# Kernel tuning notes

Measured on AMD Instinct MI355X. Metric: run time of the kernel, lower is better.

## Reference

```python
import jax, jax.numpy as jnp
import numpy as np

H = 16  # num_heads


def rope_cos_sin(S, d):
    # interleaved RoPE tables: cos = [cos0,cos0,cos1,cos1,...], sin likewise
    pos = jnp.arange(S, dtype=jnp.float32)[:, None]            # [S,1]
    ids = jnp.arange(d // 2, dtype=jnp.float32)
    theta = jnp.power(10000.0, -2.0 * ids / d)                  # [d/2]
    ang = pos * theta                                           # [S,d/2]
    cos = jnp.repeat(jnp.cos(ang), 2, axis=-1)                  # [S,d]
    sin = jnp.repeat(jnp.sin(ang), 2, axis=-1)                  # [S,d]
    return cos, sin


def apply_rope(x, cos, sin):
    # x: [B,H,S,d]; x2 = [-x1, x0, -x3, x2, ...]
    x2 = jnp.stack([-x[..., 1::2], x[..., ::2]], axis=-1).reshape(x.shape)
    return x * cos + x2 * sin


def setup_inputs() -> dict:
    key = jax.random.key(0)
    ks = jax.random.split(key, 9)
    B, S, D = 2, 2048, 1024
    sc = 1.0 / np.sqrt(D)
    return {
        "x": jax.random.normal(ks[0], (B, S, D), dtype=jnp.float32),
        "Wq": jax.random.normal(ks[1], (D, D), dtype=jnp.float32) * sc,
        "bq": jnp.zeros((D,), dtype=jnp.float32),
        "Wk": jax.random.normal(ks[2], (D, D), dtype=jnp.float32) * sc,
        "bk": jnp.zeros((D,), dtype=jnp.float32),
        "Wv": jax.random.normal(ks[3], (D, D), dtype=jnp.float32) * sc,
        "bv": jnp.zeros((D,), dtype=jnp.float32),
        "Wo": jax.random.normal(ks[4], (D, D), dtype=jnp.float32) * sc,
        "bo": jnp.zeros((D,), dtype=jnp.float32),
    }


def reference(x, Wq, bq, Wk, bk, Wv, bv, Wo, bo):
    B, S, D = x.shape
    dk = D // H
    scale = dk ** -0.5  # lsa=False -> fixed scale
    # QKV projections -> [B,H,S,dk]
    q = (x @ Wq + bq).reshape(B, S, H, dk).transpose(0, 2, 1, 3)
    k = (x @ Wk + bk).reshape(B, S, H, dk).transpose(0, 2, 1, 3)
    v = (x @ Wv + bv).reshape(B, S, H, dk).transpose(0, 2, 1, 3)
    cos, sin = rope_cos_sin(S, dk)
    q = apply_rope(q, cos, sin)
    k = apply_rope(k, cos, sin)
    attn_scores = jnp.einsum('bhqd,bhkd->bhqk', q, k) * scale
    attn_weights = jax.nn.softmax(attn_scores, axis=-1)  # dropout p=0
    out = jnp.einsum('bhqk,bhkd->bhqd', attn_weights, v)
    out = out.transpose(0, 2, 1, 3).reshape(B, S, D)
    out = out @ Wo + bo
    return out, attn_weights
```

## Files before the change

### kernel.cpp

```cpp
#include <hip/hip_runtime.h>

typedef __attribute__((ext_vector_type(4))) float f32x4;
typedef __attribute__((ext_vector_type(4))) int   i32x4;
typedef __attribute__((ext_vector_type(8))) short bf16x8;
typedef __attribute__((ext_vector_type(4))) short s16x4;

#define HD 16
#define SQ 2048
#define DM 1024
#define DK 64
#define QSCALE 0.18033688011112042f

__device__ __forceinline__ short f2bf(float f){
  union { float f; unsigned u; } c; c.f = f;
  unsigned r = (c.u + 0x7FFFu + ((c.u >> 16) & 1u)) >> 16;
  return (short)r;
}
__device__ __forceinline__ f32x4 mfma16(bf16x8 a, bf16x8 b, f32x4 c){
  return __builtin_amdgcn_mfma_f32_16x16x32_bf16(a, b, c, 0, 0, 0);
}
__device__ __forceinline__ void gload16(const void* g, void* l){
  __builtin_amdgcn_global_load_lds(
      (const __attribute__((address_space(1))) unsigned*)g,
      (__attribute__((address_space(3))) unsigned*)l, 16, 0, 0);
}


__global__ void k_rope_tab(float2* __restrict__ tab){
  int i = blockIdx.x * 256 + threadIdx.x;
  int s = i >> 5, d2 = i & 31;
  float theta = powf(10000.0f, -(float)d2 / 32.0f);
  float ang = (float)s * theta;
  tab[i] = make_float2(cosf(ang), sinf(ang));
}

__global__ void k_cast(const float* __restrict__ x, short* __restrict__ xb){
  int i = (blockIdx.x * 256 + threadIdx.x) * 4;
  f32x4 v = *(const f32x4*)(x + i);
  s16x4 o;
  o[0] = f2bf(v[0]); o[1] = f2bf(v[1]); o[2] = f2bf(v[2]); o[3] = f2bf(v[3]);
  *(s16x4*)(xb + i) = o;
}

__global__ void k_wt4(const float* __restrict__ W0, const float* __restrict__ W1,
                      const float* __restrict__ W2, const float* __restrict__ W3,
                      short* __restrict__ T0, short* __restrict__ T1,
                      short* __restrict__ T2, short* __restrict__ T3){
  __shared__ float t[32][33];
  const float* W; short* Wt;
  if (blockIdx.z == 0)      { W = W0; Wt = T0; }
  else if (blockIdx.z == 1) { W = W1; Wt = T1; }
  else if (blockIdx.z == 2) { W = W2; Wt = T2; }
  else                      { W = W3; Wt = T3; }
  int kx = blockIdx.x * 32, nx = blockIdx.y * 32;
  int lx = threadIdx.x & 31, ly = threadIdx.x >> 5;
#pragma unroll
  for (int i = 0; i < 32; i += 8)
    t[ly + i][lx] = W[(size_t)(kx + ly + i) * DM + nx + lx];
  __syncthreads();
#pragma unroll
  for (int i = 0; i < 32; i += 8)
    Wt[(size_t)(nx + ly + i) * DM + kx + lx] = f2bf(t[lx][ly + i]);
}

__global__ __launch_bounds__(256) void k_projqkv(const short* __restrict__ A,
    const short* __restrict__ Wqt, const short* __restrict__ Wkt, const short* __restrict__ Wvt,
    const float* __restrict__ bq, const float* __restrict__ bk, const float* __restrict__ bv,
    const float2* __restrict__ rope,
    short* __restrict__ Qo, short* __restrict__ Ko, short* __restrict__ Vo)
{
  __shared__ short As[128 * 64];
  __shared__ short Bs[128 * 64];
  const int mat = blockIdx.y >> 3;
  const int n0 = (blockIdx.y & 7) * 128;
  const short* Bt  = (mat == 0) ? Wqt : (mat == 1) ? Wkt : Wvt;
  const float* bias = (mat == 0) ? bq : (mat == 1) ? bk : bv;
  const int tid = threadIdx.x;
  const int lane = tid & 63, w = tid >> 6;
  const int wr = w >> 1, wc = w & 1;
  const int l15 = lane & 15, l4 = lane >> 4;
  const int m0 = blockIdx.x * 128;
  f32x4 acc[4][4] = {};

  for (int k0 = 0; k0 < DM; k0 += 64) {
#pragma unroll
    for (int i = 0; i < 4; ++i) {
      int c = w * 4 + i;
      int row = c * 8 + (lane >> 3);
      int so = (((lane & 7) * 16) ^ ((row & 7) << 4)) >> 1;
      gload16(A  + (size_t)(m0 + row) * DM + k0 + so, (char*)As + c * 1024);
      gload16(Bt + (size_t)(n0 + row) * DM + k0 + so, (char*)Bs + c * 1024);
    }
    __syncthreads();
#pragma unroll
    for (int kk = 0; kk < 64; kk += 32) {
      bf16x8 af[4], bfr[4];
#pragma unroll
      for (int mi = 0; mi < 4; ++mi) {
        int r = wr * 64 + mi * 16 + l15;
        af[mi] = *(const bf16x8*)((char*)As + ((r * 128 + kk * 2 + l4 * 16) ^ ((r & 7) << 4)));
      }
#pragma unroll
      for (int ni = 0; ni < 4; ++ni) {
        int r = wc * 64 + ni * 16 + l15;
        bfr[ni] = *(const bf16x8*)((char*)Bs + ((r * 128 + kk * 2 + l4 * 16) ^ ((r & 7) << 4)));
      }
#pragma unroll
      for (int mi = 0; mi < 4; ++mi)
#pragma unroll
        for (int ni = 0; ni < 4; ++ni)
          acc[mi][ni] = mfma16(af[mi], bfr[ni], acc[mi][ni]);
    }
    __syncthreads();
  }

#pragma unroll
  for (int mi = 0; mi < 4; ++mi) {
#pragma unroll
    for (int ni = 0; ni < 4; ++ni) {
      int n = n0 + wc * 64 + ni * 16 + l15;
      float bv2 = bias[n];
      if (mat == 2) {
        s16x4 pk;
        int mb = m0 + wr * 64 + mi * 16 + l4 * 4;
#pragma unroll
        for (int r2 = 0; r2 < 4; ++r2) pk[r2] = f2bf(acc[mi][ni][r2] + bv2);
        int b = mb >> 11, s = mb & 2047, h = n >> 6, d = n & 63;
        *(s16x4*)(Vo + ((size_t)((b * HD + h) * DK + d)) * SQ + s) = pk;
      } else {
        short* outp = (mat == 0) ? Qo : Ko;
        float sc = (mat == 0) ? QSCALE : 1.0f;
#pragma unroll
        for (int r2 = 0; r2 < 4; ++r2) {
          int m = m0 + wr * 64 + mi * 16 + l4 * 4 + r2;
          float v = acc[mi][ni][r2] + bv2;
          float pr = __shfl_xor(v, 1);
          int s = m & 2047, d = n & 63;
          float2 cs = rope[(s << 5) + (d >> 1)];
          v = (d & 1) ? (v * cs.x + pr * cs.y) : (v * cs.x - pr * cs.y);
          v *= sc;
          int b = m >> 11, h = n >> 6;
          outp[((size_t)((b * HD + h) * SQ + s)) * DK + d] = f2bf(v);
        }
      }
    }
  }
}

__global__ __launch_bounds__(256) void k_projO(const short* __restrict__ A, const short* __restrict__ Bt,
                                               const float* __restrict__ bias, float* __restrict__ out)
{
  __shared__ short As[64 * 64];
  __shared__ short Bs[128 * 64];
  const int tid = threadIdx.x;
  const int lane = tid & 63, w = tid >> 6;
  const int wr = w >> 1, wc = w & 1;
  const int l15 = lane & 15, l4 = lane >> 4;
  const int m0 = blockIdx.x * 64, n0 = blockIdx.y * 128;
  f32x4 acc[2][4] = {};

  for (int k0 = 0; k0 < DM; k0 += 64) {
#pragma unroll
    for (int i = 0; i < 2; ++i) {
      int c = w * 2 + i;
      int row = c * 8 + (lane >> 3);
      int so = (((lane & 7) * 16) ^ ((row & 7) << 4)) >> 1;
      gload16(A + (size_t)(m0 + row) * DM + k0 + so, (char*)As + c * 1024);
    }
#pragma unroll
    for (int i = 0; i < 4; ++i) {
      int c = w * 4 + i;
      int row = c * 8 + (lane >> 3);
      int so = (((lane & 7) * 16) ^ ((row & 7) << 4)) >> 1;
      gload16(Bt + (size_t)(n0 + row) * DM + k0 + so, (char*)Bs + c * 1024);
    }
    __syncthreads();
#pragma unroll
    for (int kk = 0; kk < 64; kk += 32) {
      bf16x8 af[2], bfr[4];
#pragma unroll
      for (int mi = 0; mi < 2; ++mi) {
        int r = wr * 32 + mi * 16 + l15;
        af[mi] = *(const bf16x8*)((char*)As + ((r * 128 + kk * 2 + l4 * 16) ^ ((r & 7) << 4)));
      }
#pragma unroll
      for (int ni = 0; ni < 4; ++ni) {
        int r = wc * 64 + ni * 16 + l15;
        bfr[ni] = *(const bf16x8*)((char*)Bs + ((r * 128 + kk * 2 + l4 * 16) ^ ((r & 7) << 4)));
      }
#pragma unroll
      for (int mi = 0; mi < 2; ++mi)
#pragma unroll
        for (int ni = 0; ni < 4; ++ni)
          acc[mi][ni] = mfma16(af[mi], bfr[ni], acc[mi][ni]);
    }
    __syncthreads();
  }

#pragma unroll
  for (int mi = 0; mi < 2; ++mi)
#pragma unroll
    for (int ni = 0; ni < 4; ++ni) {
      int n = n0 + wc * 64 + ni * 16 + l15;
      float bv2 = bias[n];
#pragma unroll
      for (int r2 = 0; r2 < 4; ++r2) {
        int m = m0 + wr * 32 + mi * 16 + l4 * 4 + r2;
        out[(size_t)m * DM + n] = acc[mi][ni][r2] + bv2;
      }
    }
}

__global__ __launch_bounds__(256, 4) void k_attn2(const short* __restrict__ Q, const short* __restrict__ K,
    const short* __restrict__ Vt, float* __restrict__ attn_out, short* __restrict__ ctx)
{
  __shared__ short Kbuf[2][64 * 64];
  __shared__ short Vbuf[2][64 * 64];
  __shared__ short Ps[64 * 64];
  const int idx = blockIdx.x;
  const int xcd = idx & 7, g = idx >> 3;
  const int bh = xcd * 4 + (g >> 5);
  const int qt = g & 31;
  const int tid = threadIdx.x, lane = tid & 63, w = tid >> 6;
  const int l15 = lane & 15, l4 = lane >> 4;
  const int qg = w >> 1, kg = w & 1;
  const short* Qg = Q + (size_t)(bh * SQ + qt * 64) * DK;
  const short* Kg = K + (size_t)bh * SQ * DK;
  const short* Vg = Vt + (size_t)bh * DK * SQ;

  const int c0 = w * 2, c1 = w * 2 + 1;
  const int row0 = c0 * 8 + (lane >> 3), row1 = c1 * 8 + (lane >> 3);
  const int so0 = (((lane & 7) * 16) ^ ((row0 & 7) << 4)) >> 1;
  const int so1 = (((lane & 7) * 16) ^ ((row1 & 7) << 4)) >> 1;

  bf16x8 q_b[2][2];
#pragma unroll
  for (int qs = 0; qs < 2; ++qs)
#pragma unroll
    for (int kx = 0; kx < 2; ++kx)
      q_b[qs][kx] = *(const bf16x8*)(Qg + (qg * 32 + qs * 16 + l15) * 64 + kx * 32 + l4 * 8);

  gload16(Kg + (size_t)row0 * 64 + so0, (char*)Kbuf[0] + c0 * 1024);
  gload16(Kg + (size_t)row1 * 64 + so1, (char*)Kbuf[0] + c1 * 1024);
  __syncthreads();
  float rs[2] = {0.0f, 0.0f};
  for (int t = 0; t < 32; ++t) {
    int cur = t & 1;
    if (t < 31) {
      gload16(Kg + (size_t)((t + 1) * 64 + row0) * 64 + so0, (char*)Kbuf[cur ^ 1] + c0 * 1024);
      gload16(Kg + (size_t)((t + 1) * 64 + row1) * 64 + so1, (char*)Kbuf[cur ^ 1] + c1 * 1024);
    }
    const char* Kc = (const char*)Kbuf[cur];
    bf16x8 af[2][2];
#pragma unroll
    for (int ks = 0; ks < 2; ++ks)
#pragma unroll
      for (int kx = 0; kx < 2; ++kx) {
        int r = kg * 32 + ks * 16 + l15;
        af[ks][kx] = *(const bf16x8*)(Kc + ((r * 128 + kx * 64 + l4 * 16) ^ ((r & 7) << 4)));
      }
#pragma unroll
    for (int qs = 0; qs < 2; ++qs)
#pragma unroll
      for (int ks = 0; ks < 2; ++ks) {
        f32x4 p = {};
        p = mfma16(af[ks][0], q_b[qs][0], p);
        p = mfma16(af[ks][1], q_b[qs][1], p);
#pragma unroll
        for (int r2 = 0; r2 < 4; ++r2) rs[qs] += exp2f(p[r2]);
      }
    __syncthreads();
  }
  float rv[2];
#pragma unroll
  for (int qs = 0; qs < 2; ++qs) {
    float v = rs[qs];
    v += __shfl_xor(v, 16);
    v += __shfl_xor(v, 32);
    rv[qs] = v;
  }
  {
    float* rst = (float*)Ps;
    if (lane < 16) {
#pragma unroll
      for (int qs = 0; qs < 2; ++qs)
        rst[(((qg * 2 + qs) * 16 + l15) * 2) + kg] = rv[qs];
    }
    __syncthreads();
#pragma unroll
    for (int qs = 0; qs < 2; ++qs)
      rv[qs] = 1.0f / (rv[qs] + rst[(((qg * 2 + qs) * 16 + l15) * 2) + (kg ^ 1)]);
  }
  const float rinv0 = rv[0], rinv1 = rv[1];

  f32x4 c[2][4] = {};
  float* attn_base = attn_out + ((size_t)(bh * SQ + qt * 64)) * SQ;

  gload16(Kg + (size_t)row0 * 64 + so0, (char*)Kbuf[0] + c0 * 1024);
  gload16(Kg + (size_t)row1 * 64 + so1, (char*)Kbuf[0] + c1 * 1024);
  gload16(Vg + (size_t)row0 * SQ + so0, (char*)Vbuf[0] + c0 * 1024);
  gload16(Vg + (size_t)row1 * SQ + so1, (char*)Vbuf[0] + c1 * 1024);
  __syncthreads();
  for (int t = 0; t < 32; ++t) {
    int cur = t & 1;
    if (t < 31) {
      gload16(Kg + (size_t)((t + 1) * 64 + row0) * 64 + so0, (char*)Kbuf[cur ^ 1] + c0 * 1024);
      gload16(Kg + (size_t)((t + 1) * 64 + row1) * 64 + so1, (char*)Kbuf[cur ^ 1] + c1 * 1024);
      gload16(Vg + (size_t)row0 * SQ + (t + 1) * 64 + so0, (char*)Vbuf[cur ^ 1] + c0 * 1024);
      gload16(Vg + (size_t)row1 * SQ + (t + 1) * 64 + so1, (char*)Vbuf[cur ^ 1] + c1 * 1024);
    }
    const char* Kc = (const char*)Kbuf[cur];
    const char* Vc = (const char*)Vbuf[cur];
    bf16x8 af[2][2];
#pragma unroll
    for (int ks = 0; ks < 2; ++ks)
#pragma unroll
      for (int kx = 0; kx < 2; ++kx) {
        int r = kg * 32 + ks * 16 + l15;
        af[ks][kx] = *(const bf16x8*)(Kc + ((r * 128 + kx * 64 + l4 * 16) ^ ((r & 7) << 4)));
      }
#pragma unroll
    for (int qs = 0; qs < 2; ++qs) {
      const float rinv = qs ? rinv1 : rinv0;
#pragma unroll
      for (int ks = 0; ks < 2; ++ks) {
        f32x4 p = {};
        p = mfma16(af[ks][0], q_b[qs][0], p);
        p = mfma16(af[ks][1], q_b[qs][1], p);
        f32x4 wv;
        s16x4 pk;
#pragma unroll
        for (int r2 = 0; r2 < 4; ++r2) {
          wv[r2] = exp2f(p[r2]) * rinv;
          pk[r2] = f2bf(wv[r2]);
        }
        int qr = qg * 32 + qs * 16 + l15;
        *(f32x4*)(attn_base + (size_t)qr * SQ + t * 64 + kg * 32 + ks * 16 + l4 * 4) = wv;
        *(s16x4*)((char*)Ps + ((qr * 128 + kg * 64 + ks * 32 + l4 * 8) ^ ((qr & 7) << 4))) = pk;
      }
    }
#pragma unroll
    for (int qs = 0; qs < 2; ++qs) {
      int qr = qg * 32 + qs * 16 + l15;
      bf16x8 ap = *(const bf16x8*)((char*)Ps + ((qr * 128 + kg * 64 + l4 * 16) ^ ((qr & 7) << 4)));
#pragma unroll
      for (int ds = 0; ds < 4; ++ds) {
        int r = ds * 16 + l15;
        bf16x8 bv = *(const bf16x8*)(Vc + ((r * 128 + kg * 64 + l4 * 16) ^ ((r & 7) << 4)));
        c[qs][ds] = mfma16(ap, bv, c[qs][ds]);
      }
    }
    __syncthreads();
  }
  float* red = (float*)Kbuf;
  if (kg == 1) {
#pragma unroll
    for (int qs = 0; qs < 2; ++qs)
#pragma unroll
      for (int ds = 0; ds < 4; ++ds)
#pragma unroll
        for (int r2 = 0; r2 < 4; ++r2)
          red[(qg * 32 + qs * 16 + l4 * 4 + r2) * 64 + ds * 16 + l15] = c[qs][ds][r2];
  }
  __syncthreads();
  if (kg == 0) {
    int b = bh >> 4, h = bh & 15;
#pragma unroll
    for (int qs = 0; qs < 2; ++qs)
#pragma unroll
      for (int ds = 0; ds < 4; ++ds)
#pragma unroll
        for (int r2 = 0; r2 < 4; ++r2) {
          int qr = qg * 32 + qs * 16 + l4 * 4 + r2;
          float v = c[qs][ds][r2] + red[qr * 64 + ds * 16 + l15];
          int s = qt * 64 + qr, d = ds * 16 + l15;
          ctx[((size_t)(b * SQ + s)) * DM + h * DK + d] = f2bf(v);
        }
  }
}

extern "C" void kernel_launch(void* const* d_in, const int* in_sizes, int n_in,
                              void* d_out, int out_size, void* d_ws, size_t ws_size,
                              hipStream_t stream)
{
  const float* x  = (const float*)d_in[0];
  const float* Wq = (const float*)d_in[1];
  const float* bq = (const float*)d_in[2];
  const float* Wk = (const float*)d_in[3];
  const float* bk = (const float*)d_in[4];
  const float* Wv = (const float*)d_in[5];
  const float* bv = (const float*)d_in[6];
  const float* Wo = (const float*)d_in[7];
  const float* bo = (const float*)d_in[8];

  char* p = (char*)d_ws;
  float2* rope = (float2*)p;  p += (size_t)SQ * 32 * sizeof(float2);
  short* xb  = (short*)p;     p += (size_t)4096 * DM * 2;
  short* Wqt = (short*)p;     p += (size_t)DM * DM * 2;
  short* Wkt = (short*)p;     p += (size_t)DM * DM * 2;
  short* Wvt = (short*)p;     p += (size_t)DM * DM * 2;
  short* Wot = (short*)p;     p += (size_t)DM * DM * 2;
  short* Qr  = (short*)p;     p += (size_t)2 * HD * SQ * DK * 2;
  short* Kr  = (short*)p;     p += (size_t)2 * HD * SQ * DK * 2;
  short* Vtr = (short*)p;     p += (size_t)2 * HD * SQ * DK * 2;
  short* ctx = (short*)p;     p += (size_t)4096 * DM * 2;

  k_rope_tab<<<SQ * 32 / 256, 256, 0, stream>>>(rope);
  k_cast<<<4096 * DM / 1024, 256, 0, stream>>>(x, xb);
  k_wt4<<<dim3(32, 32, 4), 256, 0, stream>>>(Wq, Wk, Wv, Wo, Wqt, Wkt, Wvt, Wot);
  k_projqkv<<<dim3(32, 24), 256, 0, stream>>>(xb, Wqt, Wkt, Wvt, bq, bk, bv, rope, Qr, Kr, Vtr);
  float* attn = (float*)d_out + (size_t)2 * SQ * DM;
  k_attn2<<<1024, 256, 0, stream>>>(Qr, Kr, Vtr, attn, ctx);
  k_projO<<<dim3(64, 8), 256, 0, stream>>>(ctx, Wot, bo, (float*)d_out);
}
```

Measured before the change: 283.1 us.

## Stage attention weights in LDS for coalesced stores; fuse prep kernels

The attention kernel now double-buffers the bf16 probability tile in LDS. It writes the previous tile's attention weights to global memory as contiguous row segments, one step later, instead of scattered per-lane fp32 stores. This targets the large attn_weights write. The returned weights are now bf16-rounded values widened back to fp32, and LDS use grows, so launch bounds drop from 4 to 3 blocks per SM. The first softmax pass processes two K tiles per barrier, and the rope, cast and weight-transpose kernels are merged into a single launch.

```diff
diff --git a/kernel.cpp b/kernel.cpp
--- a/kernel.cpp
+++ b/kernel.cpp
@@ -16,6 +16,10 @@
   unsigned r = (c.u + 0x7FFFu + ((c.u >> 16) & 1u)) >> 16;
   return (short)r;
 }
+__device__ __forceinline__ float bf2f(short s){
+  union { unsigned u; float f; } c; c.u = ((unsigned)(unsigned short)s) << 16;
+  return c.f;
+}
 __device__ __forceinline__ f32x4 mfma16(bf16x8 a, bf16x8 b, f32x4 c){
   return __builtin_amdgcn_mfma_f32_16x16x32_bf16(a, b, c, 0, 0, 0);
 }
@@ -25,42 +29,43 @@
       (__attribute__((address_space(3))) unsigned*)l, 16, 0, 0);
 }
 
-
-__global__ void k_rope_tab(float2* __restrict__ tab){
-  int i = blockIdx.x * 256 + threadIdx.x;
-  int s = i >> 5, d2 = i & 31;
-  float theta = powf(10000.0f, -(float)d2 / 32.0f);
-  float ang = (float)s * theta;
-  tab[i] = make_float2(cosf(ang), sinf(ang));
-}
-
-__global__ void k_cast(const float* __restrict__ x, short* __restrict__ xb){
-  int i = (blockIdx.x * 256 + threadIdx.x) * 4;
-  f32x4 v = *(const f32x4*)(x + i);
-  s16x4 o;
-  o[0] = f2bf(v[0]); o[1] = f2bf(v[1]); o[2] = f2bf(v[2]); o[3] = f2bf(v[3]);
-  *(s16x4*)(xb + i) = o;
-}
-
-__global__ void k_wt4(const float* __restrict__ W0, const float* __restrict__ W1,
-                      const float* __restrict__ W2, const float* __restrict__ W3,
-                      short* __restrict__ T0, short* __restrict__ T1,
-                      short* __restrict__ T2, short* __restrict__ T3){
+__global__ void k_prep(const float* __restrict__ x, short* __restrict__ xb,
+    const float* __restrict__ W0, const float* __restrict__ W1,
+    const float* __restrict__ W2, const float* __restrict__ W3,
+    short* __restrict__ T0, short* __restrict__ T1,
+    short* __restrict__ T2, short* __restrict__ T3,
+    float2* __restrict__ rope)
+{
   __shared__ float t[32][33];
-  const float* W; short* Wt;
-  if (blockIdx.z == 0)      { W = W0; Wt = T0; }
-  else if (blockIdx.z == 1) { W = W1; Wt = T1; }
-  else if (blockIdx.z == 2) { W = W2; Wt = T2; }
-  else                      { W = W3; Wt = T3; }
-  int kx = blockIdx.x * 32, nx = blockIdx.y * 32;
-  int lx = threadIdx.x & 31, ly = threadIdx.x >> 5;
-#pragma unroll
-  for (int i = 0; i < 32; i += 8)
-    t[ly + i][lx] = W[(size_t)(kx + ly + i) * DM + nx + lx];
-  __syncthreads();
-#pragma unroll
-  for (int i = 0; i < 32; i += 8)
-    Wt[(size_t)(nx + ly + i) * DM + kx + lx] = f2bf(t[lx][ly + i]);
+  const int bid = blockIdx.x, tid = threadIdx.x;
+  if (bid < 4096) {
+    int i = (bid * 256 + tid) * 4;
+    f32x4 v = *(const f32x4*)(x + i);
+    s16x4 o;
+    o[0] = f2bf(v[0]); o[1] = f2bf(v[1]); o[2] = f2bf(v[2]); o[3] = f2bf(v[3]);
+    *(s16x4*)(xb + i) = o;
+  } else if (bid < 8192) {
+    int rem = bid - 4096;
+    int z = rem >> 10, rxy = rem & 1023;
+    int bx = rxy & 31, by = rxy >> 5;
+    const float* W = (z == 0) ? W0 : (z == 1) ? W1 : (z == 2) ? W2 : W3;
+    short* Wt = (z == 0) ? T0 : (z == 1) ? T1 : (z == 2) ? T2 : T3;
+    int kx = bx * 32, nx = by * 32;
+    int lx = tid & 31, ly = tid >> 5;
+#pragma unroll
+    for (int i2 = 0; i2 < 32; i2 += 8)
+      t[ly + i2][lx] = W[(size_t)(kx + ly + i2) * DM + nx + lx];
+    __syncthreads();
+#pragma unroll
+    for (int i2 = 0; i2 < 32; i2 += 8)
+      Wt[(size_t)(nx + ly + i2) * DM + kx + lx] = f2bf(t[lx][ly + i2]);
+  } else {
+    int i = (bid - 8192) * 256 + tid;
+    int s = i >> 5, d2 = i & 31;
+    float theta = powf(10000.0f, -(float)d2 / 32.0f);
+    float ang = (float)s * theta;
+    rope[i] = make_float2(cosf(ang), sinf(ang));
+  }
 }
 
 __global__ __launch_bounds__(256) void k_projqkv(const short* __restrict__ A,
@@ -211,12 +216,11 @@
     }
 }
 
-__global__ __launch_bounds__(256, 4) void k_attn2(const short* __restrict__ Q, const short* __restrict__ K,
+__global__ __launch_bounds__(256, 3) void k_attn2(const short* __restrict__ Q, const short* __restrict__ K,
     const short* __restrict__ Vt, float* __restrict__ attn_out, short* __restrict__ ctx)
 {
-  __shared__ short Kbuf[2][64 * 64];
-  __shared__ short Vbuf[2][64 * 64];
-  __shared__ short Ps[64 * 64];
+  __shared__ short KV4[4][64 * 64];
+  __shared__ short Ps2[2][64 * 64];
   const int idx = blockIdx.x;
   const int xcd = idx & 7, g = idx >> 3;
   const int bh = xcd * 4 + (g >> 5);
@@ -227,6 +231,7 @@
   const short* Qg = Q + (size_t)(bh * SQ + qt * 64) * DK;
   const short* Kg = K + (size_t)bh * SQ * DK;
   const short* Vg = Vt + (size_t)bh * DK * SQ;
+  char* KVb = (char*)KV4;
 
   const int c0 = w * 2, c1 = w * 2 + 1;
   const int row0 = c0 * 8 + (lane >> 3), row1 = c1 * 8 + (lane >> 3);
@@ -240,35 +245,43 @@
     for (int kx = 0; kx < 2; ++kx)
       q_b[qs][kx] = *(const bf16x8*)(Qg + (qg * 32 + qs * 16 + l15) * 64 + kx * 32 + l4 * 8);
 
-  gload16(Kg + (size_t)row0 * 64 + so0, (char*)Kbuf[0] + c0 * 1024);
-  gload16(Kg + (size_t)row1 * 64 + so1, (char*)Kbuf[0] + c1 * 1024);
+  gload16(Kg + (size_t)row0 * 64 + so0, KVb + 0 * 8192 + c0 * 1024);
+  gload16(Kg + (size_t)row1 * 64 + so1, KVb + 0 * 8192 + c1 * 1024);
+  gload16(Kg + (size_t)(64 + row0) * 64 + so0, KVb + 1 * 8192 + c0 * 1024);
+  gload16(Kg + (size_t)(64 + row1) * 64 + so1, KVb + 1 * 8192 + c1 * 1024);
   __syncthreads();
   float rs[2] = {0.0f, 0.0f};
-  for (int t = 0; t < 32; ++t) {
-    int cur = t & 1;
-    if (t < 31) {
-      gload16(Kg + (size_t)((t + 1) * 64 + row0) * 64 + so0, (char*)Kbuf[cur ^ 1] + c0 * 1024);
-      gload16(Kg + (size_t)((t + 1) * 64 + row1) * 64 + so1, (char*)Kbuf[cur ^ 1] + c1 * 1024);
-    }
-    const char* Kc = (const char*)Kbuf[cur];
-    bf16x8 af[2][2];
-#pragma unroll
-    for (int ks = 0; ks < 2; ++ks)
-#pragma unroll
-      for (int kx = 0; kx < 2; ++kx) {
-        int r = kg * 32 + ks * 16 + l15;
-        af[ks][kx] = *(const bf16x8*)(Kc + ((r * 128 + kx * 64 + l4 * 16) ^ ((r & 7) << 4)));
-      }
-#pragma unroll
-    for (int qs = 0; qs < 2; ++qs)
-#pragma unroll
-      for (int ks = 0; ks < 2; ++ks) {
-        f32x4 p = {};
-        p = mfma16(af[ks][0], q_b[qs][0], p);
-        p = mfma16(af[ks][1], q_b[qs][1], p);
-#pragma unroll
-        for (int r2 = 0; r2 < 4; ++r2) rs[qs] += exp2f(p[r2]);
-      }
+  for (int i = 0; i < 16; ++i) {
+    int cur = (i & 1) * 2;
+    if (i < 15) {
+      int nb = (i + 1) * 128, ns = cur ^ 2;
+      gload16(Kg + (size_t)(nb + row0) * 64 + so0, KVb + ns * 8192 + c0 * 1024);
+      gload16(Kg + (size_t)(nb + row1) * 64 + so1, KVb + ns * 8192 + c1 * 1024);
+      gload16(Kg + (size_t)(nb + 64 + row0) * 64 + so0, KVb + (ns + 1) * 8192 + c0 * 1024);
+      gload16(Kg + (size_t)(nb + 64 + row1) * 64 + so1, KVb + (ns + 1) * 8192 + c1 * 1024);
+    }
+#pragma unroll
+    for (int sl = 0; sl < 2; ++sl) {
+      const char* Kc = KVb + (cur + sl) * 8192;
+      bf16x8 af[2][2];
+#pragma unroll
+      for (int ks = 0; ks < 2; ++ks)
+#pragma unroll
+        for (int kx = 0; kx < 2; ++kx) {
+          int r = kg * 32 + ks * 16 + l15;
+          af[ks][kx] = *(const bf16x8*)(Kc + ((r * 128 + kx * 64 + l4 * 16) ^ ((r & 7) << 4)));
+        }
+#pragma unroll
+      for (int qs = 0; qs < 2; ++qs)
+#pragma unroll
+        for (int ks = 0; ks < 2; ++ks) {
+          f32x4 p = {};
+          p = mfma16(af[ks][0], q_b[qs][0], p);
+          p = mfma16(af[ks][1], q_b[qs][1], p);
+#pragma unroll
+          for (int r2 = 0; r2 < 4; ++r2) rs[qs] += exp2f(p[r2]);
+        }
+    }
     __syncthreads();
   }
   float rv[2];
@@ -280,7 +293,7 @@
     rv[qs] = v;
   }
   {
-    float* rst = (float*)Ps;
+    float* rst = (float*)Ps2[0];
     if (lane < 16) {
 #pragma unroll
       for (int qs = 0; qs < 2; ++qs)
@@ -295,22 +308,36 @@
 
   f32x4 c[2][4] = {};
   float* attn_base = attn_out + ((size_t)(bh * SQ + qt * 64)) * SQ;
-
-  gload16(Kg + (size_t)row0 * 64 + so0, (char*)Kbuf[0] + c0 * 1024);
-  gload16(Kg + (size_t)row1 * 64 + so1, (char*)Kbuf[0] + c1 * 1024);
-  gload16(Vg + (size_t)row0 * SQ + so0, (char*)Vbuf[0] + c0 * 1024);
-  gload16(Vg + (size_t)row1 * SQ + so1, (char*)Vbuf[0] + c1 * 1024);
+  const int wb_r = tid >> 2, wb_cc = tid & 3;
+  const int wb_sw = (wb_r & 7) << 4;
+
+  gload16(Kg + (size_t)row0 * 64 + so0, KVb + 0 * 8192 + c0 * 1024);
+  gload16(Kg + (size_t)row1 * 64 + so1, KVb + 0 * 8192 + c1 * 1024);
+  gload16(Vg + (size_t)row0 * SQ + so0, KVb + 2 * 8192 + c0 * 1024);
+  gload16(Vg + (size_t)row1 * SQ + so1, KVb + 2 * 8192 + c1 * 1024);
   __syncthreads();
   for (int t = 0; t < 32; ++t) {
     int cur = t & 1;
     if (t < 31) {
-      gload16(Kg + (size_t)((t + 1) * 64 + row0) * 64 + so0, (char*)Kbuf[cur ^ 1] + c0 * 1024);
-      gload16(Kg + (size_t)((t + 1) * 64 + row1) * 64 + so1, (char*)Kbuf[cur ^ 1] + c1 * 1024);
-      gload16(Vg + (size_t)row0 * SQ + (t + 1) * 64 + so0, (char*)Vbuf[cur ^ 1] + c0 * 1024);
-      gload16(Vg + (size_t)row1 * SQ + (t + 1) * 64 + so1, (char*)Vbuf[cur ^ 1] + c1 * 1024);
-    }
-    const char* Kc = (const char*)Kbuf[cur];
-    const char* Vc = (const char*)Vbuf[cur];
+      gload16(Kg + (size_t)((t + 1) * 64 + row0) * 64 + so0, KVb + (cur ^ 1) * 8192 + c0 * 1024);
+      gload16(Kg + (size_t)((t + 1) * 64 + row1) * 64 + so1, KVb + (cur ^ 1) * 8192 + c1 * 1024);
+      gload16(Vg + (size_t)row0 * SQ + (t + 1) * 64 + so0, KVb + (2 + (cur ^ 1)) * 8192 + c0 * 1024);
+      gload16(Vg + (size_t)row1 * SQ + (t + 1) * 64 + so1, KVb + (2 + (cur ^ 1)) * 8192 + c1 * 1024);
+    }
+    if (t > 0) {
+      const char* Pp = (const char*)Ps2[cur ^ 1];
+      float* dst = attn_base + (size_t)wb_r * SQ + (t - 1) * 64 + wb_cc * 16;
+#pragma unroll
+      for (int j = 0; j < 4; ++j) {
+        s16x4 pv = *(const s16x4*)(Pp + ((wb_r * 128 + wb_cc * 32 + j * 8) ^ wb_sw));
+        f32x4 o;
+        o[0] = bf2f(pv[0]); o[1] = bf2f(pv[1]); o[2] = bf2f(pv[2]); o[3] = bf2f(pv[3]);
+        *(f32x4*)(dst + j * 4) = o;
+      }
+    }
+    const char* Kc = KVb + cur * 8192;
+    const char* Vc = KVb + (2 + cur) * 8192;
+    char* Pc = (char*)Ps2[cur];
     bf16x8 af[2][2];
 #pragma unroll
     for (int ks = 0; ks < 2; ++ks)
@@ -327,22 +354,18 @@
         f32x4 p = {};
         p = mfma16(af[ks][0], q_b[qs][0], p);
         p = mfma16(af[ks][1], q_b[qs][1], p);
-        f32x4 wv;
         s16x4 pk;
 #pragma unroll
-        for (int r2 = 0; r2 < 4; ++r2) {
-          wv[r2] = exp2f(p[r2]) * rinv;
-          pk[r2] = f2bf(wv[r2]);
-        }
+        for (int r2 = 0; r2 < 4; ++r2)
+          pk[r2] = f2bf(exp2f(p[r2]) * rinv);
         int qr = qg * 32 + qs * 16 + l15;
-        *(f32x4*)(attn_base + (size_t)qr * SQ + t * 64 + kg * 32 + ks * 16 + l4 * 4) = wv;
-        *(s16x4*)((char*)Ps + ((qr * 128 + kg * 64 + ks * 32 + l4 * 8) ^ ((qr & 7) << 4))) = pk;
+        *(s16x4*)(Pc + ((qr * 128 + kg * 64 + ks * 32 + l4 * 8) ^ ((qr & 7) << 4))) = pk;
       }
     }
 #pragma unroll
     for (int qs = 0; qs < 2; ++qs) {
       int qr = qg * 32 + qs * 16 + l15;
-      bf16x8 ap = *(const bf16x8*)((char*)Ps + ((qr * 128 + kg * 64 + l4 * 16) ^ ((qr & 7) << 4)));
+      bf16x8 ap = *(const bf16x8*)(Pc + ((qr * 128 + kg * 64 + l4 * 16) ^ ((qr & 7) << 4)));
 #pragma unroll
       for (int ds = 0; ds < 4; ++ds) {
         int r = ds * 16 + l15;
@@ -352,7 +375,18 @@
     }
     __syncthreads();
   }
-  float* red = (float*)Kbuf;
+  {
+    const char* Pp = (const char*)Ps2[1];
+    float* dst = attn_base + (size_t)wb_r * SQ + 31 * 64 + wb_cc * 16;
+#pragma unroll
+    for (int j = 0; j < 4; ++j) {
+      s16x4 pv = *(const s16x4*)(Pp + ((wb_r * 128 + wb_cc * 32 + j * 8) ^ wb_sw));
+      f32x4 o;
+      o[0] = bf2f(pv[0]); o[1] = bf2f(pv[1]); o[2] = bf2f(pv[2]); o[3] = bf2f(pv[3]);
+      *(f32x4*)(dst + j * 4) = o;
+    }
+  }
+  float* red = (float*)KV4;
   if (kg == 1) {
 #pragma unroll
     for (int qs = 0; qs < 2; ++qs)
@@ -405,9 +439,7 @@
   short* Vtr = (short*)p;     p += (size_t)2 * HD * SQ * DK * 2;
   short* ctx = (short*)p;     p += (size_t)4096 * DM * 2;
 
-  k_rope_tab<<<SQ * 32 / 256, 256, 0, stream>>>(rope);
-  k_cast<<<4096 * DM / 1024, 256, 0, stream>>>(x, xb);
-  k_wt4<<<dim3(32, 32, 4), 256, 0, stream>>>(Wq, Wk, Wv, Wo, Wqt, Wkt, Wvt, Wot);
+  k_prep<<<8448, 256, 0, stream>>>(x, xb, Wq, Wk, Wv, Wo, Wqt, Wkt, Wvt, Wot, rope);
   k_projqkv<<<dim3(32, 24), 256, 0, stream>>>(xb, Wqt, Wkt, Wvt, bq, bk, bv, rope, Qr, Kr, Vtr);
   float* attn = (float*)d_out + (size_t)2 * SQ * DM;
   k_attn2<<<1024, 256, 0, stream>>>(Qr, Kr, Vtr, attn, ctx);
```

After: 332.4 us. 17.4% more time.
